# Performance work log

Measured on AMD Instinct MI355X. Metric: run time of the kernel, lower is better.

## Reference

```python
import jax, jax.numpy as jnp
import numpy as np

# BlendParams / camera defaults (pytorch3d)
SIGMA = 1e-4
GAMMA = 1e-4
ZNEAR = 1.0
ZFAR = 100.0
EPS_BLEND = 1e-10
BG = jnp.array([1.0, 1.0, 1.0], dtype=jnp.float32)

N, H, W, K = 8, 512, 512, 4
V, F = 50000, 100000


def _normalize(x, eps=1e-6):
    n = jnp.linalg.norm(x, axis=-1, keepdims=True)
    return x / jnp.maximum(n, eps)


def setup_inputs() -> dict:
    key = jax.random.key(0)
    ks = jax.random.split(key, 12)
    verts = jax.random.normal(ks[0], (V, 3), jnp.float32)
    vertex_normals = _normalize(jax.random.normal(ks[1], (V, 3), jnp.float32))
    faces = jax.random.randint(ks[2], (F, 3), 0, V)
    p2f = jax.random.randint(ks[3], (N, H, W, K), 0, F)
    drop = jax.random.uniform(ks[4], (N, H, W, K)) < 0.2
    pix_to_face = jnp.where(drop, -1, p2f)
    bary = jax.random.uniform(ks[5], (N, H, W, K, 3), jnp.float32, 1e-3, 1.0)
    bary_coords = bary / bary.sum(-1, keepdims=True)  # valid barycentric weights
    zbuf = jax.random.uniform(ks[6], (N, H, W, K), jnp.float32, ZNEAR, ZFAR)
    dists = jax.random.normal(ks[7], (N, H, W, K), jnp.float32) * 1e-3
    texels = jax.random.uniform(ks[8], (N, H, W, K, 3), jnp.float32)
    vis_maps = jax.random.uniform(ks[9], (N, H, W, 3), jnp.float32)
    light_location = jax.random.normal(ks[10], (N, 3), jnp.float32) * 3.0
    camera_center = jax.random.normal(ks[11], (N, 3), jnp.float32) * 5.0
    return dict(
        verts=verts, vertex_normals=vertex_normals, bary_coords=bary_coords,
        zbuf=zbuf, dists=dists, texels=texels, vis_maps=vis_maps,
        light_location=light_location,
        light_ambient=jnp.full((N, 3), 0.5, jnp.float32),
        light_diffuse=jnp.full((N, 3), 0.3, jnp.float32),
        light_specular=jnp.full((N, 3), 0.2, jnp.float32),
        camera_center=camera_center,
        mat_ambient=jnp.ones((N, 3), jnp.float32),
        mat_diffuse=jnp.ones((N, 3), jnp.float32),
        mat_specular=jnp.ones((N, 3), jnp.float32),
        shininess=jnp.full((N,), 64.0, jnp.float32),
        faces=faces, pix_to_face=pix_to_face,
    )


def _interpolate_face_attributes(pix_to_face, bary, face_attrs):
    # face_attrs: (F, 3, D); pix_to_face: (N,H,W,K); bary: (N,H,W,K,3)
    mask = pix_to_face < 0
    idx = jnp.where(mask, 0, pix_to_face)
    gathered = face_attrs[idx]  # (N,H,W,K,3,D)
    out = jnp.einsum('nhwkv,nhwkvd->nhwkd', bary, gathered)
    return jnp.where(mask[..., None], 0.0, out)


def reference(verts, vertex_normals, bary_coords, zbuf, dists, texels, vis_maps,
              light_location, light_ambient, light_diffuse, light_specular,
              camera_center, mat_ambient, mat_diffuse, mat_specular, shininess,
              faces, pix_to_face):
    faces_verts = verts[faces]            # (F,3,3)
    faces_normals = vertex_normals[faces]  # (F,3,3)
    pixel_coords = _interpolate_face_attributes(pix_to_face, bary_coords, faces_verts)
    pixel_normals = _interpolate_face_attributes(pix_to_face, bary_coords, faces_normals)

    # ---- Phong lighting (PointLights) ----
    b = lambda v: v[:, None, None, None, :]  # (N,3) -> (N,1,1,1,3)
    normals = _normalize(pixel_normals)
    direction = _normalize(b(light_location) - pixel_coords)
    cos_angle = jnp.sum(normals * direction, axis=-1)  # (N,H,W,K)
    diffuse_light = b(light_diffuse) * jax.nn.relu(cos_angle)[..., None]
    reflect = -direction + 2.0 * cos_angle[..., None] * normals
    view_dir = _normalize(b(camera_center) - pixel_coords)
    spec_cos = jax.nn.relu(jnp.sum(view_dir * reflect, axis=-1)) * (cos_angle > 0)
    spec_light = b(light_specular) * (spec_cos ** shininess[:, None, None, None])[..., None]
    ambient = b(mat_ambient * light_ambient)
    diffuse = b(mat_diffuse) * diffuse_light
    specular = b(mat_specular) * spec_light

    vis = vis_maps[:, :, :, None, :]  # broadcast over K (== unsqueeze(-2).repeat)
    colors = (ambient + diffuse * vis) * texels + specular  # (N,H,W,K,3)

    # ---- softmax_rgb_blend ----
    mask = (pix_to_face >= 0).astype(colors.dtype)
    prob_map = jax.nn.sigmoid(-dists / SIGMA) * mask
    alpha = 1.0 - jnp.prod(1.0 - prob_map, axis=-1)
    z_inv = (ZFAR - zbuf) / (ZFAR - ZNEAR) * mask
    z_inv_max = jnp.maximum(jnp.max(z_inv, axis=-1, keepdims=True), EPS_BLEND)
    weights_num = prob_map * jnp.exp((z_inv - z_inv_max) / GAMMA)
    delta = jnp.exp((EPS_BLEND - z_inv_max) / GAMMA)
    denom = jnp.sum(weights_num, axis=-1, keepdims=True) + delta
    weighted_colors = jnp.einsum('nhwk,nhwkc->nhwc', weights_num, colors)
    rgb = (weighted_colors + delta * BG) / denom
    return jnp.concatenate([rgb, alpha[..., None]], axis=-1)  # (N,H,W,4)
```

## Files before the change

kernel.cpp:

```cpp
#include <hip/hip_runtime.h>
#include <math.h>

#define SIGMA_C   1e-4f
#define GAMMA_C   1e-4f
#define ZNEAR_C   1.0f
#define ZFAR_C    100.0f
#define EPSB_C    1e-10f
#define INV_SIGMA  (1.0f / SIGMA_C)
#define INV_GAMMA  (1.0f / GAMMA_C)
#define INV_ZRANGE (1.0f / (ZFAR_C - ZNEAR_C))

static constexpr int N_ = 8, H_ = 512, W_ = 512, K_ = 4;
static constexpr int NPIX = N_ * H_ * W_;
static constexpr int NSMP = NPIX * K_;
static constexpr int F_ = 100000;
static constexpr int REC_U = 16;
static constexpr size_t TABLE_BYTES = (size_t)F_ * REC_U * sizeof(unsigned int);
static_assert((H_ * W_ * K_) / 256 == 4096, "uniform-n derivation");

typedef float        fvec4 __attribute__((ext_vector_type(4)));
typedef float        fvec2 __attribute__((ext_vector_type(2)));
typedef unsigned int uvec4 __attribute__((ext_vector_type(4)));
typedef unsigned int uvec2 __attribute__((ext_vector_type(2)));
typedef _Float16     hvec2 __attribute__((ext_vector_type(2)));
typedef float        fvec3_ __attribute__((ext_vector_type(3)));
typedef fvec3_       fvec3 __attribute__((aligned(4)));

struct F3 { float x, y, z; };

__device__ __forceinline__ float ntf(const float* p) {
    return __builtin_nontemporal_load(p);
}
__device__ __forceinline__ fvec3_ ntf3(const float* p) {
    return __builtin_nontemporal_load(reinterpret_cast<const fvec3*>(p));
}
__device__ __forceinline__ unsigned int packh(float lo, float hi) {
    hvec2 h; h.x = (_Float16)lo; h.y = (_Float16)hi;
    return __builtin_bit_cast(unsigned int, h);
}
__device__ __forceinline__ hvec2 unpackh(unsigned int u) {
    return __builtin_bit_cast(hvec2, u);
}

__device__ __forceinline__ float qxor1(float v) {
    return __builtin_bit_cast(float, __builtin_amdgcn_update_dpp(
        0, __builtin_bit_cast(int, v), 0xB1, 0xF, 0xF, true));
}
__device__ __forceinline__ float qxor2(float v) {
    return __builtin_bit_cast(float, __builtin_amdgcn_update_dpp(
        0, __builtin_bit_cast(int, v), 0x4E, 0xF, 0xF, true));
}
__device__ __forceinline__ float qbc0(float v) {
    return __builtin_bit_cast(float, __builtin_amdgcn_update_dpp(
        0, __builtin_bit_cast(int, v), 0x00, 0xF, 0xF, true));
}
__device__ __forceinline__ float qbc1(float v) {
    return __builtin_bit_cast(float, __builtin_amdgcn_update_dpp(
        0, __builtin_bit_cast(int, v), 0x55, 0xF, 0xF, true));
}
__device__ __forceinline__ float qbc2(float v) {
    return __builtin_bit_cast(float, __builtin_amdgcn_update_dpp(
        0, __builtin_bit_cast(int, v), 0xAA, 0xF, 0xF, true));
}

__device__ __forceinline__ float frcp(float x)  { return __builtin_amdgcn_rcpf(x); }
__device__ __forceinline__ float frsq(float x)  { return __builtin_amdgcn_rsqf(x); }

__global__ __launch_bounds__(256) void build_face_table(
    const float* __restrict__ verts,
    const float* __restrict__ vnorm,
    const int*   __restrict__ faces,
    unsigned int* __restrict__ table)
{
    const int f = blockIdx.x * 256 + threadIdx.x;
    if (f >= F_) return;
    const int i0 = faces[3*f+0], i1 = faces[3*f+1], i2 = faces[3*f+2];
    const F3 a = reinterpret_cast<const F3*>(verts)[i0];
    const F3 b = reinterpret_cast<const F3*>(verts)[i1];
    const F3 c = reinterpret_cast<const F3*>(verts)[i2];
    const F3 p = reinterpret_cast<const F3*>(vnorm)[i0];
    const F3 q = reinterpret_cast<const F3*>(vnorm)[i1];
    const F3 r = reinterpret_cast<const F3*>(vnorm)[i2];
    unsigned int* o = table + (size_t)f * REC_U;
    fvec4 A; A.x = p.x; A.y = p.y; A.z = p.z; A.w = q.x;
    fvec4 B; B.x = q.y; B.y = q.z; B.z = r.x; B.w = r.y;
    uvec4 C; C.x = __builtin_bit_cast(unsigned int, r.z);
    C.y = packh(a.x, a.y); C.z = packh(a.z, b.x); C.w = packh(b.y, b.z);
    uvec4 D; D.x = packh(c.x, c.y); D.y = packh(c.z, 0.0f); D.z = 0u; D.w = 0u;
    *reinterpret_cast<fvec4*>(o + 0)  = A;
    *reinterpret_cast<fvec4*>(o + 4)  = B;
    *reinterpret_cast<uvec4*>(o + 8)  = C;
    *reinterpret_cast<uvec4*>(o + 12) = D;
}

__global__ __launch_bounds__(256) void soft_phong_sample(
    const unsigned int* __restrict__ table,
    const float* __restrict__ bary,
    const float* __restrict__ zbuf,
    const float* __restrict__ dists,
    const float* __restrict__ texels,
    const float* __restrict__ vis,
    const float* __restrict__ l_loc,
    const float* __restrict__ l_amb,
    const float* __restrict__ l_dif,
    const float* __restrict__ l_spec,
    const float* __restrict__ cam,
    const float* __restrict__ m_amb,
    const float* __restrict__ m_dif,
    const float* __restrict__ m_spec,
    const float* __restrict__ shininess,
    const int*   __restrict__ p2f,
    float* __restrict__ out)
{
    const int s = blockIdx.x * 256 + threadIdx.x;
    const int p = s >> 2;
    const int k = s & 3;
    const int n = blockIdx.x >> 12;

    const int  f0   = __builtin_nontemporal_load(p2f + s);
    const bool live = f0 >= 0;
    const int  f    = live ? f0 : 0;
    const unsigned int* rec = table + (size_t)f * REC_U;
    const fvec4 A = *reinterpret_cast<const fvec4*>(rec + 0);
    const fvec4 B = *reinterpret_cast<const fvec4*>(rec + 4);
    const uvec4 C = *reinterpret_cast<const uvec4*>(rec + 8);
    const uvec2 D = *reinterpret_cast<const uvec2*>(rec + 12);

    const float  zb = ntf(zbuf + s);
    const float  dd = ntf(dists + s);
    const fvec3_ bv = ntf3(bary + 3*s);
    const fvec3_ tv = ntf3(texels + 3*s);
    const float b0 = bv.x, b1 = bv.y, b2 = bv.z;
    const float t0 = tv.x, t1 = tv.y, t2 = tv.z;

    const int   kv = (k < 3) ? k : 2;
    const float lv = vis[3*p + kv];
    const float vR = qbc0(lv), vG = qbc1(lv), vB = qbc2(lv);

    const float llx = l_loc[3*n+0], lly = l_loc[3*n+1], llz = l_loc[3*n+2];
    const float ccx = cam[3*n+0],   ccy = cam[3*n+1],   ccz = cam[3*n+2];
    const float ambR = m_amb[3*n+0]*l_amb[3*n+0];
    const float ambG = m_amb[3*n+1]*l_amb[3*n+1];
    const float ambB = m_amb[3*n+2]*l_amb[3*n+2];
    const float kdR  = m_dif[3*n+0]*l_dif[3*n+0];
    const float kdG  = m_dif[3*n+1]*l_dif[3*n+1];
    const float kdB  = m_dif[3*n+2]*l_dif[3*n+2];
    const float ksR  = m_spec[3*n+0]*l_spec[3*n+0];
    const float ksG  = m_spec[3*n+1]*l_spec[3*n+1];
    const float ksB  = m_spec[3*n+2]*l_spec[3*n+2];
    const float shin = shininess[n];

    const float n2z = __builtin_bit_cast(float, C.x);
    const hvec2 h0 = unpackh(C.y);
    const hvec2 h1 = unpackh(C.z);
    const hvec2 h2 = unpackh(C.w);
    const hvec2 h3 = unpackh(D.x);
    const hvec2 h4 = unpackh(D.y);
    const float v0x = (float)h0.x, v0y = (float)h0.y, v0z = (float)h1.x;
    const float v1x = (float)h1.y, v1y = (float)h2.x, v1z = (float)h2.y;
    const float v2x = (float)h3.x, v2y = (float)h3.y, v2z = (float)h4.x;

    const float pcx = b0*v0x + b1*v1x + b2*v2x;
    const float pcy = b0*v0y + b1*v1y + b2*v2y;
    const float pcz = b0*v0z + b1*v1z + b2*v2z;

    const float pnx = b0*A.x + b1*A.w + b2*B.z;
    const float pny = b0*A.y + b1*B.x + b2*B.w;
    const float pnz = b0*A.z + b1*B.y + b2*n2z;

    const float inl = frsq(fmaxf(pnx*pnx + pny*pny + pnz*pnz, 1e-12f));
    const float nx = pnx*inl, ny = pny*inl, nz = pnz*inl;

    float dx = llx - pcx, dy = lly - pcy, dz = llz - pcz;
    const float idl = frsq(fmaxf(dx*dx + dy*dy + dz*dz, 1e-12f));
    dx *= idl; dy *= idl; dz *= idl;

    const float cosang = nx*dx + ny*dy + nz*dz;
    const float rcos   = fmaxf(cosang, 0.0f);

    const float rx = 2.0f*cosang*nx - dx;
    const float ry = 2.0f*cosang*ny - dy;
    const float rz = 2.0f*cosang*nz - dz;

    float vx = ccx - pcx, vy = ccy - pcy, vz = ccz - pcz;
    const float ivl = frsq(fmaxf(vx*vx + vy*vy + vz*vz, 1e-12f));
    vx *= ivl; vy *= ivl; vz *= ivl;

    const float sdot = vx*rx + vy*ry + vz*rz;
    const float spec_cos = (cosang > 0.0f) ? fmaxf(sdot, 0.0f) : 0.0f;
    const float sp = (spec_cos > 0.0f) ? exp2f(shin * log2f(spec_cos)) : 0.0f;

    const float colR = (ambR + kdR*rcos*vR) * t0 + ksR*sp;
    const float colG = (ambG + kdG*rcos*vG) * t1 + ksG*sp;
    const float colB = (ambB + kdB*rcos*vB) * t2 + ksB*sp;

    const float prob = live ? frcp(1.0f + __expf(dd * INV_SIGMA)) : 0.0f;
    const float zinv = live ? (ZFAR_C - zb) * INV_ZRANGE : 0.0f;

    float zmax = zinv;
    zmax = fmaxf(zmax, qxor1(zmax));
    zmax = fmaxf(zmax, qxor2(zmax));
    zmax = fmaxf(zmax, EPSB_C);

    const float w = prob * __expf((zinv - zmax) * INV_GAMMA);
    float aw = w, aR = w*colR, aG = w*colG, aB = w*colB, kp = 1.0f - prob;

    aw += qxor1(aw);  aR += qxor1(aR);
    aG += qxor1(aG);  aB += qxor1(aB);
    kp *= qxor1(kp);
    aw += qxor2(aw);  aR += qxor2(aR);
    aG += qxor2(aG);  aB += qxor2(aB);
    kp *= qxor2(kp);

    const float delta = __expf((EPSB_C - zmax) * INV_GAMMA);
    const float inv   = frcp(aw + delta);

    float val;
    if      (k == 0) val = (aR + delta) * inv;
    else if (k == 1) val = (aG + delta) * inv;
    else if (k == 2) val = (aB + delta) * inv;
    else             val = 1.0f - kp;
    __builtin_nontemporal_store(val, out + s);
}

__global__ __launch_bounds__(256) void soft_phong_direct(
    const float* __restrict__ verts,
    const float* __restrict__ vnorm,
    const float* __restrict__ bary,
    const float* __restrict__ zbuf,
    const float* __restrict__ dists,
    const float* __restrict__ texels,
    const float* __restrict__ vis,
    const float* __restrict__ l_loc,
    const float* __restrict__ l_amb,
    const float* __restrict__ l_dif,
    const float* __restrict__ l_spec,
    const float* __restrict__ cam,
    const float* __restrict__ m_amb,
    const float* __restrict__ m_dif,
    const float* __restrict__ m_spec,
    const float* __restrict__ shininess,
    const int*   __restrict__ faces,
    const int*   __restrict__ p2f,
    float* __restrict__ out)
{
    const int p = blockIdx.x * 256 + threadIdx.x;
    const int n = p >> 18;
    struct I3 { int x, y, z; };
    const int fi[4] = {p2f[4*p+0], p2f[4*p+1], p2f[4*p+2], p2f[4*p+3]};
    I3 fidx[4];
#pragma unroll
    for (int k = 0; k < 4; ++k) {
        const int f = (fi[k] >= 0) ? fi[k] : 0;
        fidx[k] = reinterpret_cast<const I3*>(faces)[f];
    }
    F3 vp[4][3], vn[4][3];
#pragma unroll
    for (int k = 0; k < 4; ++k) {
        const int i0 = fidx[k].x, i1 = fidx[k].y, i2 = fidx[k].z;
        vp[k][0] = reinterpret_cast<const F3*>(verts)[i0];
        vp[k][1] = reinterpret_cast<const F3*>(verts)[i1];
        vp[k][2] = reinterpret_cast<const F3*>(verts)[i2];
        vn[k][0] = reinterpret_cast<const F3*>(vnorm)[i0];
        vn[k][1] = reinterpret_cast<const F3*>(vnorm)[i1];
        vn[k][2] = reinterpret_cast<const F3*>(vnorm)[i2];
    }
    const float llx = l_loc[3*n+0], lly = l_loc[3*n+1], llz = l_loc[3*n+2];
    const float ccx = cam[3*n+0],   ccy = cam[3*n+1],   ccz = cam[3*n+2];
    const float ambR = m_amb[3*n+0]*l_amb[3*n+0];
    const float ambG = m_amb[3*n+1]*l_amb[3*n+1];
    const float ambB = m_amb[3*n+2]*l_amb[3*n+2];
    const float kdR  = m_dif[3*n+0]*l_dif[3*n+0];
    const float kdG  = m_dif[3*n+1]*l_dif[3*n+1];
    const float kdB  = m_dif[3*n+2]*l_dif[3*n+2];
    const float ksR  = m_spec[3*n+0]*l_spec[3*n+0];
    const float ksG  = m_spec[3*n+1]*l_spec[3*n+1];
    const float ksB  = m_spec[3*n+2]*l_spec[3*n+2];
    const float shin = shininess[n];
    float colR[4], colG[4], colB[4], prob[4], zinv[4];
    float zmax = EPSB_C;
#pragma unroll
    for (int k = 0; k < 4; ++k) {
        const bool live = fi[k] >= 0;
        const float b0 = bary[12*p+3*k+0], b1 = bary[12*p+3*k+1], b2 = bary[12*p+3*k+2];
        const float pcx = b0*vp[k][0].x + b1*vp[k][1].x + b2*vp[k][2].x;
        const float pcy = b0*vp[k][0].y + b1*vp[k][1].y + b2*vp[k][2].y;
        const float pcz = b0*vp[k][0].z + b1*vp[k][1].z + b2*vp[k][2].z;
        const float pnx = b0*vn[k][0].x + b1*vn[k][1].x + b2*vn[k][2].x;
        const float pny = b0*vn[k][0].y + b1*vn[k][1].y + b2*vn[k][2].y;
        const float pnz = b0*vn[k][0].z + b1*vn[k][1].z + b2*vn[k][2].z;
        const float inl = frsq(fmaxf(pnx*pnx + pny*pny + pnz*pnz, 1e-12f));
        const float nx = pnx*inl, ny = pny*inl, nz = pnz*inl;
        float dx = llx - pcx, dy = lly - pcy, dz = llz - pcz;
        const float idl = frsq(fmaxf(dx*dx + dy*dy + dz*dz, 1e-12f));
        dx *= idl; dy *= idl; dz *= idl;
        const float cosang = nx*dx + ny*dy + nz*dz;
        const float rcos   = fmaxf(cosang, 0.0f);
        const float rx = 2.0f*cosang*nx - dx;
        const float ry = 2.0f*cosang*ny - dy;
        const float rz = 2.0f*cosang*nz - dz;
        float vx = ccx - pcx, vy = ccy - pcy, vz = ccz - pcz;
        const float ivl = frsq(fmaxf(vx*vx + vy*vy + vz*vz, 1e-12f));
        vx *= ivl; vy *= ivl; vz *= ivl;
        const float sdot = vx*rx + vy*ry + vz*rz;
        const float spec_cos = (cosang > 0.0f) ? fmaxf(sdot, 0.0f) : 0.0f;
        const float sp = (spec_cos > 0.0f) ? exp2f(shin * log2f(spec_cos)) : 0.0f;
        const float vRl = vis[3*p+0], vGl = vis[3*p+1], vBl = vis[3*p+2];
        colR[k] = (ambR + kdR*rcos*vRl) * texels[12*p+3*k+0] + ksR*sp;
        colG[k] = (ambG + kdG*rcos*vGl) * texels[12*p+3*k+1] + ksG*sp;
        colB[k] = (ambB + kdB*rcos*vBl) * texels[12*p+3*k+2] + ksB*sp;
        prob[k] = live ? frcp(1.0f + __expf(dists[4*p+k] * INV_SIGMA)) : 0.0f;
        zinv[k] = live ? (ZFAR_C - zbuf[4*p+k]) * INV_ZRANGE : 0.0f;
        zmax = fmaxf(zmax, zinv[k]);
    }
    const float delta = __expf((EPSB_C - zmax) * INV_GAMMA);
    float denom = delta, accR = delta, accG = delta, accB = delta, keep = 1.0f;
#pragma unroll
    for (int k = 0; k < 4; ++k) {
        const float w = prob[k] * __expf((zinv[k] - zmax) * INV_GAMMA);
        denom += w; accR += w*colR[k]; accG += w*colG[k]; accB += w*colB[k];
        keep *= (1.0f - prob[k]);
    }
    const float inv = frcp(denom);
    out[4*p+0] = accR*inv; out[4*p+1] = accG*inv; out[4*p+2] = accB*inv; out[4*p+3] = 1.0f - keep;
}

extern "C" void kernel_launch(void* const* d_in, const int* in_sizes, int n_in,
                              void* d_out, int out_size, void* d_ws, size_t ws_size,
                              hipStream_t stream) {
    const float* verts   = (const float*)d_in[0];
    const float* vnorm   = (const float*)d_in[1];
    const float* bary    = (const float*)d_in[2];
    const float* zbuf    = (const float*)d_in[3];
    const float* dists   = (const float*)d_in[4];
    const float* texels  = (const float*)d_in[5];
    const float* vis     = (const float*)d_in[6];
    const float* l_loc   = (const float*)d_in[7];
    const float* l_amb   = (const float*)d_in[8];
    const float* l_dif   = (const float*)d_in[9];
    const float* l_spec  = (const float*)d_in[10];
    const float* cam     = (const float*)d_in[11];
    const float* m_amb   = (const float*)d_in[12];
    const float* m_dif   = (const float*)d_in[13];
    const float* m_spec  = (const float*)d_in[14];
    const float* shin    = (const float*)d_in[15];
    const int*   faces   = (const int*)d_in[16];
    const int*   p2f     = (const int*)d_in[17];
    float* out = (float*)d_out;

    if (ws_size >= TABLE_BYTES) {
        unsigned int* table = (unsigned int*)d_ws;
        build_face_table<<<(F_ + 255) / 256, 256, 0, stream>>>(verts, vnorm, faces, table);
        soft_phong_sample<<<NSMP / 256, 256, 0, stream>>>(
            table, bary, zbuf, dists, texels, vis,
            l_loc, l_amb, l_dif, l_spec, cam,
            m_amb, m_dif, m_spec, shin, p2f, out);
    } else {
        soft_phong_direct<<<NPIX / 256, 256, 0, stream>>>(
            verts, vnorm, bary, zbuf, dists, texels, vis,
            l_loc, l_amb, l_dif, l_spec, cam,
            m_amb, m_dif, m_spec, shin, faces, p2f, out);
    }
}
```

Measured before the change: 359.7 us.

## Cooperatively gather face records across quad lanes and transpose through LDS

Each quad of four threads now broadcasts its four face indices with DPP. Every lane then loads one 16-byte chunk of each of the four 64-byte face records, so each record is fetched by contiguous lanes as a coalesced unit. The chunks are written to a padded LDS buffer and read back so each thread gets its full record. This replaces four scattered 16-byte loads per thread with grouped loads, at the cost of LDS traffic and extra instructions. No barrier is used, which relies on quad lanes being in the same wavefront.

```diff
diff --git a/kernel.cpp b/kernel.cpp
--- a/kernel.cpp
+++ b/kernel.cpp
@@ -61,6 +61,18 @@
 __device__ __forceinline__ float qbc2(float v) {
     return __builtin_bit_cast(float, __builtin_amdgcn_update_dpp(
         0, __builtin_bit_cast(int, v), 0xAA, 0xF, 0xF, true));
+}
+__device__ __forceinline__ int qbci0(int v) {
+    return __builtin_amdgcn_update_dpp(0, v, 0x00, 0xF, 0xF, true);
+}
+__device__ __forceinline__ int qbci1(int v) {
+    return __builtin_amdgcn_update_dpp(0, v, 0x55, 0xF, 0xF, true);
+}
+__device__ __forceinline__ int qbci2(int v) {
+    return __builtin_amdgcn_update_dpp(0, v, 0xAA, 0xF, 0xF, true);
+}
+__device__ __forceinline__ int qbci3(int v) {
+    return __builtin_amdgcn_update_dpp(0, v, 0xFF, 0xF, 0xF, true);
 }
 
 __device__ __forceinline__ float frcp(float x)  { return __builtin_amdgcn_rcpf(x); }
@@ -112,29 +124,45 @@
     const int*   __restrict__ p2f,
     float* __restrict__ out)
 {
-    const int s = blockIdx.x * 256 + threadIdx.x;
+    __shared__ unsigned int xlds[64 * 80];
+
+    const int tid = threadIdx.x;
+    const int s = blockIdx.x * 256 + tid;
     const int p = s >> 2;
-    const int k = s & 3;
+    const int k = tid & 3;
+    const int tq = tid >> 2;
     const int n = blockIdx.x >> 12;
 
     const int  f0   = __builtin_nontemporal_load(p2f + s);
     const bool live = f0 >= 0;
     const int  f    = live ? f0 : 0;
-    const unsigned int* rec = table + (size_t)f * REC_U;
-    const fvec4 A = *reinterpret_cast<const fvec4*>(rec + 0);
-    const fvec4 B = *reinterpret_cast<const fvec4*>(rec + 4);
-    const uvec4 C = *reinterpret_cast<const uvec4*>(rec + 8);
-    const uvec2 D = *reinterpret_cast<const uvec2*>(rec + 12);
+
+    const int fb0 = qbci0(f), fb1 = qbci1(f), fb2 = qbci2(f), fb3 = qbci3(f);
+
+    const uvec4 r0 = *reinterpret_cast<const uvec4*>(table + (size_t)fb0 * REC_U + 4*k);
+    const uvec4 r1 = *reinterpret_cast<const uvec4*>(table + (size_t)fb1 * REC_U + 4*k);
+    const uvec4 r2 = *reinterpret_cast<const uvec4*>(table + (size_t)fb2 * REC_U + 4*k);
+    const uvec4 r3 = *reinterpret_cast<const uvec4*>(table + (size_t)fb3 * REC_U + 4*k);
 
     const float  zb = ntf(zbuf + s);
     const float  dd = ntf(dists + s);
     const fvec3_ bv = ntf3(bary + 3*s);
     const fvec3_ tv = ntf3(texels + 3*s);
+    const int   kv = (k < 3) ? k : 2;
+    const float lv = vis[3*p + kv];
+
+    unsigned int* qb = xlds + tq * 80;
+    *reinterpret_cast<uvec4*>(qb + 0*20 + 4*k) = r0;
+    *reinterpret_cast<uvec4*>(qb + 1*20 + 4*k) = r1;
+    *reinterpret_cast<uvec4*>(qb + 2*20 + 4*k) = r2;
+    *reinterpret_cast<uvec4*>(qb + 3*20 + 4*k) = r3;
+    const fvec4 A = *reinterpret_cast<const fvec4*>(qb + k*20 + 0);
+    const fvec4 B = *reinterpret_cast<const fvec4*>(qb + k*20 + 4);
+    const uvec4 C = *reinterpret_cast<const uvec4*>(qb + k*20 + 8);
+    const uvec2 D = *reinterpret_cast<const uvec2*>(qb + k*20 + 12);
+
     const float b0 = bv.x, b1 = bv.y, b2 = bv.z;
     const float t0 = tv.x, t1 = tv.y, t2 = tv.z;
-
-    const int   kv = (k < 3) ? k : 2;
-    const float lv = vis[3*p + kv];
     const float vR = qbc0(lv), vG = qbc1(lv), vB = qbc2(lv);
 
     const float llx = l_loc[3*n+0], lly = l_loc[3*n+1], llz = l_loc[3*n+2];
```

Result: no change. 353.8 us (-1.6%).
